# Kernel tuning notes

Measured on AMD Instinct MI355X. Metric: run time of the kernel, lower is better.

The kernel has to match this reference:

```python
import jax, jax.numpy as jnp
import numpy as np

N_NODES = 50000
N_EDGES = 800000
C = 128
NEG_SLOPE = 0.01  # nn.LeakyReLU default


def _init_linear(key, fan_in, fan_out):
    kw, kb = jax.random.split(key)
    lim = 1.0 / np.sqrt(fan_in)
    W = jax.random.uniform(kw, (fan_in, fan_out), jnp.float32, -lim, lim)
    b = jax.random.uniform(kb, (fan_out,), jnp.float32, -lim, lim)
    return W, b


def setup_inputs() -> dict:
    key = jax.random.key(0)
    ks = jax.random.split(key, 10)
    x = jax.random.normal(ks[0], (N_NODES, C), jnp.float32)
    pos = jax.random.normal(ks[1], (N_NODES, 3), jnp.float32)
    edge_index = jax.random.randint(ks[2], (2, N_EDGES), 0, N_NODES, jnp.int64)
    # mlp_h: Linear(C,C) -> LeakyReLU -> Linear(C,3) -> Tanh
    Wh1, bh1 = _init_linear(ks[3], C, C)
    Wh2, bh2 = _init_linear(ks[4], C, 3)
    # mlp_f: Linear(C+3, C) -> LeakyReLU
    Wf, bf = _init_linear(ks[5], C + 3, C)
    # mlp_g: Linear(C,C) -> LeakyReLU -> Linear(C,C)
    Wg1, bg1 = _init_linear(ks[6], C, C)
    Wg2, bg2 = _init_linear(ks[7], C, C)
    return {"x": x, "pos": pos, "edge_index": edge_index,
            "Wh1": Wh1, "bh1": bh1, "Wh2": Wh2, "bh2": bh2,
            "Wf": Wf, "bf": bf,
            "Wg1": Wg1, "bg1": bg1, "Wg2": Wg2, "bg2": bg2}


def reference(x, pos, edge_index, Wh1, bh1, Wh2, bh2, Wf, bf, Wg1, bg1, Wg2, bg2):
    lrelu = lambda t: jax.nn.leaky_relu(t, NEG_SLOPE)
    # delta_i = tanh(mlp_h(x_i))  -> [N, 3]
    delta = jnp.tanh(lrelu(x @ Wh1 + bh1) @ Wh2 + bh2)
    src, dst = edge_index[0], edge_index[1]  # message j -> i (PyG convention)
    # per-edge relative position: pos_j - pos_i + delta_i  -> [E, 3]
    rel = pos[src] - pos[dst] + delta[dst]
    # per-edge message: mlp_f([rel, x_j])  -> [E, C]
    e = lrelu(jnp.concatenate([rel, x[src]], axis=-1) @ Wf + bf)
    # scatter-max aggregate over incoming edges per target node
    agg = jax.ops.segment_max(e, dst, num_segments=N_NODES)
    agg = jnp.where(jnp.isfinite(agg), agg, 0.0)  # empty segments -> 0
    # out_i = mlp_g(agg_i) + x_i
    out = lrelu(agg @ Wg1 + bg1) @ Wg2 + bg2 + x
    return out
```

## Files before the change

### kernel.cpp

```cpp
#include <hip/hip_runtime.h>
#include <cfloat>
#include <cmath>

#define NEG_SLOPE 0.01f

typedef __attribute__((ext_vector_type(8))) short short8;
typedef __attribute__((ext_vector_type(4))) float f32x4;

__device__ __forceinline__ float lrelu(float v) { return v >= 0.0f ? v : NEG_SLOPE * v; }

__device__ __forceinline__ ushort f2b(float f) {
    unsigned u = __float_as_uint(f);
    u += 0x7fffu + ((u >> 16) & 1u);
    return (ushort)(u >> 16);
}
__device__ __forceinline__ float b2f(ushort s) { return __uint_as_float(((unsigned)s) << 16); }

__device__ __forceinline__ void split8(const float* v, short8& hi, short8& lo) {
#pragma unroll
    for (int j = 0; j < 8; ++j) {
        ushort h = f2b(v[j]);
        hi[j] = (short)h;
        lo[j] = (short)f2b(v[j] - b2f(h));
    }
}

__global__ __launch_bounds__(256) void count_wprep_kernel(
    const int* __restrict__ ei, int* __restrict__ G, int E,
    const float* __restrict__ Wh1, const float* __restrict__ Wf,
    const float* __restrict__ Wg1, const float* __restrict__ Wg2,
    ushort* __restrict__ WT)
{
    __shared__ int cnt[256];
    const int t = threadIdx.x;
    const int b = blockIdx.x;

    {
        int tt = b * 256 + t;
        int mat = tt >> 14;
        int idx = tt & 16383;
        int n = idx >> 7, k = idx & 127;
        float v;
        if (mat == 0)      v = Wh1[k * 128 + n];
        else if (mat == 1) v = Wf[(k + 3) * 128 + n];
        else if (mat == 2) v = Wg1[k * 128 + n];
        else               v = Wg2[k * 128 + n];
        WT[(tt - idx) + n * 128 + k] = f2b(v);
    }

    cnt[t] = 0;
    __syncthreads();
    for (int e = b * 256 + t; e < E; e += 65536)
        atomicAdd(&cnt[ei[E + e] >> 8], 1);
    __syncthreads();
    G[b * 256 + t] = cnt[t];
}


#define GEMM_CORE_REG(ACC, AH, AL)                                              \
    {                                                                           \
        _Pragma("unroll")                                                       \
        for (int ks = 0; ks < 4; ++ks) {                                        \
            _Pragma("unroll")                                                   \
            for (int nt = 0; nt < 8; ++nt) {                                    \
                short8 bfr = *(const short8*)&Bs[(nt * 16 + ln) * 136 + ks * 32 + qd * 8]; \
                ACC[nt] = __builtin_amdgcn_mfma_f32_16x16x32_bf16(AL[ks], bfr, ACC[nt], 0, 0, 0); \
                ACC[nt] = __builtin_amdgcn_mfma_f32_16x16x32_bf16(AH[ks], bfr, ACC[nt], 0, 0, 0); \
            }                                                                   \
        }                                                                       \
    }

#define STAGE_B(WTP)                                                            \
    {                                                                           \
        _Pragma("unroll")                                                       \
        for (int i = 0; i < 8; ++i) {                                           \
            int c = tid + 256 * i;                                              \
            int r = c >> 4, col8 = (c & 15) * 8;                                \
            *(uint4*)&Bs[r * 136 + col8] = *(const uint4*)((WTP) + r * 128 + col8); \
        }                                                                       \
    }

__global__ __launch_bounds__(256, 4) void hy_scanpart_kernel(
    const int* __restrict__ ei, const int* __restrict__ G,
    int* __restrict__ bbase, uint* __restrict__ bpairs, int E, int GB,
    const float* __restrict__ x, const ushort* __restrict__ WT,
    const float* __restrict__ bh1, const float* __restrict__ Wh2,
    const float* __restrict__ bh2, const float* __restrict__ Wf,
    const float* __restrict__ pos, float* __restrict__ q,
    ushort* __restrict__ yb, int M)
{
    __shared__ ushort Bs[128 * 136];
    __shared__ int sp[512];
    const int tid = threadIdx.x;

    if (blockIdx.x >= GB) {
        int* s   = sp;
        int* cur = sp + 256;
        const int b = blockIdx.x - GB;
        const int t = tid;

        int cs = 0, pp = 0;
        for (int bb = 0; bb < 256; ++bb) {
            int v = G[bb * 256 + t];
            if (bb < b) pp += v;
            cs += v;
        }
        s[t] = cs;
        __syncthreads();
        for (int d = 1; d < 256; d <<= 1) {
            int a = (t >= d) ? s[t - d] : 0;
            __syncthreads();
            s[t] += a;
            __syncthreads();
        }
        int colbase = s[t] - cs;
        cur[t] = colbase + pp;
        if (b == 0) {
            bbase[t] = colbase;
            if (t == 255) bbase[256] = colbase + cs;
        }
        __syncthreads();

        for (int e = b * 256 + t; e < E; e += 65536) {
            int src = ei[e];
            int dst = ei[E + e];
            int p = atomicAdd(&cur[dst >> 8], 1);
            bpairs[p] = (uint)src | ((uint)(dst & 255) << 24);
        }
        return;
    }

    const int w = tid >> 6, L = tid & 63, qd = L >> 4, ln = L & 15;
    const int row0 = blockIdx.x * 64;
    const int arow = row0 + w * 16 + ln;

    short8 ah[4], al[4];
    {
        const float* base = x + (size_t)((arow < M) ? arow : 0) * 128 + qd * 8;
        float vb[8];
#pragma unroll
        for (int ks = 0; ks < 4; ++ks) {
            float4 v0 = make_float4(0.f, 0.f, 0.f, 0.f), v1 = v0;
            if (arow < M) {
                v0 = *(const float4*)(base + ks * 32);
                v1 = *(const float4*)(base + ks * 32 + 4);
            }
            vb[0] = v0.x; vb[1] = v0.y; vb[2] = v0.z; vb[3] = v0.w;
            vb[4] = v1.x; vb[5] = v1.y; vb[6] = v1.z; vb[7] = v1.w;
            split8(vb, ah[ks], al[ks]);
        }
    }

    STAGE_B(WT);
    __syncthreads();
    f32x4 acc1[8];
#pragma unroll
    for (int nt = 0; nt < 8; ++nt) acc1[nt] = (f32x4){0.f, 0.f, 0.f, 0.f};
    GEMM_CORE_REG(acc1, ah, al);
    __syncthreads();

    STAGE_B(WT + 16384);
    __syncthreads();
    f32x4 acc2[8];
#pragma unroll
    for (int nt = 0; nt < 8; ++nt) acc2[nt] = (f32x4){0.f, 0.f, 0.f, 0.f};
    GEMM_CORE_REG(acc2, ah, al);

    float qa0[4], qa1[4], qa2[4];
#pragma unroll
    for (int r = 0; r < 4; ++r) { qa0[r] = 0.f; qa1[r] = 0.f; qa2[r] = 0.f; }
#pragma unroll
    for (int nt = 0; nt < 8; ++nt) {
        int nn = nt * 16 + ln;
        float bias = bh1[nn];
        float w0 = Wh2[nn * 3], w1 = Wh2[nn * 3 + 1], w2 = Wh2[nn * 3 + 2];
#pragma unroll
        for (int r = 0; r < 4; ++r) {
            float h = lrelu(acc1[nt][r] + bias);
            qa0[r] += h * w0; qa1[r] += h * w1; qa2[r] += h * w2;
        }
    }

    __syncthreads();

    ushort* ysS = (ushort*)Bs;
#pragma unroll
    for (int r = 0; r < 4; ++r) {
        int m = w * 16 + qd * 4 + r;
        int gm = row0 + m;
        float p0 = 0.f, p1 = 0.f, p2 = 0.f;
        if (gm < M) { p0 = pos[gm * 3]; p1 = pos[gm * 3 + 1]; p2 = pos[gm * 3 + 2]; }
#pragma unroll
        for (int nt = 0; nt < 8; ++nt) {
            int n = nt * 16 + ln;
            ysS[m * 128 + n] = f2b(acc2[nt][r] + p0 * Wf[n] + p1 * Wf[128 + n] + p2 * Wf[256 + n]);
        }
    }
    __syncthreads();

#pragma unroll
    for (int i = 0; i < 4; ++i) {
        int c = tid + 256 * i;
        int r = c >> 4, col8 = (c & 15) * 8;
        if (row0 + r < M)
            *(uint4*)(yb + (size_t)(row0 + r) * 128 + col8) = *(const uint4*)&ysS[r * 128 + col8];
    }

#pragma unroll
    for (int r = 0; r < 4; ++r) {
#pragma unroll
        for (int d = 1; d < 16; d <<= 1) {
            qa0[r] += __shfl_xor(qa0[r], d);
            qa1[r] += __shfl_xor(qa1[r], d);
            qa2[r] += __shfl_xor(qa2[r], d);
        }
    }
#pragma unroll
    for (int r = 0; r < 4; ++r) {
        int gm = row0 + w * 16 + qd * 4 + r;
        if (ln < 3 && gm < M) {
            float sv = (ln == 0) ? qa0[r] : (ln == 1) ? qa1[r] : qa2[r];
            q[gm * 3 + ln] = tanhf(sv + bh2[ln]) - pos[gm * 3 + ln];
        }
    }
}

__global__ __launch_bounds__(256) void bucket_csr_kernel(
    const uint* __restrict__ bpairs, const int* __restrict__ bbase,
    int* __restrict__ offs, int* __restrict__ srcs, int E, int M, int NBK)
{
    __shared__ int deg[256], scn[256], cur[256];
    const int b = blockIdx.x;
    const int t = threadIdx.x;
    const int base = bbase[b];
    const int end  = bbase[b + 1];
    deg[t] = 0;
    __syncthreads();
    for (int p = base + t; p < end; p += 256)
        atomicAdd(&deg[bpairs[p] >> 24], 1);
    __syncthreads();
    scn[t] = deg[t];
    __syncthreads();
    for (int d = 1; d < 256; d <<= 1) {
        int a = (t >= d) ? scn[t - d] : 0;
        __syncthreads();
        scn[t] += a;
        __syncthreads();
    }
    int excl = scn[t] - deg[t];
    cur[t] = excl;
    int node = b * 256 + t;
    if (node < M) offs[node] = base + excl;
    if (node == M - 1 || (b == NBK - 1 && t == 255)) offs[M] = E;
    __syncthreads();
    for (int p = base + t; p < end; p += 256) {
        uint pk = bpairs[p];
        int qpos = atomicAdd(&cur[pk >> 24], 1);
        srcs[base + qpos] = (int)(pk & 0xFFFFFFu);
    }
}

__global__ __launch_bounds__(256) void agg_kernel(
    const int* __restrict__ offs, const int* __restrict__ srcs,
    const ushort* __restrict__ yb, ushort* __restrict__ aggb, int M)
{
    int wave = threadIdx.x >> 6;
    int lane = threadIdx.x & 63;
    int node = blockIdx.x * 4 + wave;
    if (node >= M) return;
    int o0 = offs[node], o1 = offs[node + 1];
    float a0 = -INFINITY, a1 = -INFINITY;
    const uint* yp = (const uint*)yb;
    int j = o0;
    for (; j + 7 < o1; j += 8) {
        uint u[8];
#pragma unroll
        for (int t = 0; t < 8; ++t)
            u[t] = yp[(size_t)srcs[j + t] * 64 + lane];
#pragma unroll
        for (int t = 0; t < 8; ++t) {
            a0 = fmaxf(a0, __uint_as_float(u[t] << 16));
            a1 = fmaxf(a1, __uint_as_float(u[t] & 0xFFFF0000u));
        }
    }
    for (; j + 3 < o1; j += 4) {
        uint u[4];
#pragma unroll
        for (int t = 0; t < 4; ++t)
            u[t] = yp[(size_t)srcs[j + t] * 64 + lane];
#pragma unroll
        for (int t = 0; t < 4; ++t) {
            a0 = fmaxf(a0, __uint_as_float(u[t] << 16));
            a1 = fmaxf(a1, __uint_as_float(u[t] & 0xFFFF0000u));
        }
    }
    for (; j < o1; ++j) {
        uint u = yp[(size_t)srcs[j] * 64 + lane];
        a0 = fmaxf(a0, __uint_as_float(u << 16));
        a1 = fmaxf(a1, __uint_as_float(u & 0xFFFF0000u));
    }
    uint pk = (__float_as_uint(a0) >> 16) | (__float_as_uint(a1) & 0xFFFF0000u);
    ((uint*)aggb)[(size_t)node * 64 + lane] = pk;
}

__global__ __launch_bounds__(256) void midout_kernel(
    const ushort* __restrict__ aggb, const float* __restrict__ qv,
    const float* __restrict__ Wf, const float* __restrict__ bfv,
    const ushort* __restrict__ Wg1T, const float* __restrict__ bg1,
    const ushort* __restrict__ Wg2T, const float* __restrict__ bg2,
    const float* __restrict__ x, float* __restrict__ out, int M)
{
    __shared__ ushort Bs[128 * 136];
    __shared__ ushort Ms[64 * 136];
    const int tid = threadIdx.x;
    const int w = tid >> 6, L = tid & 63, qd = L >> 4, ln = L & 15;
    const int row0 = blockIdx.x * 64;
    const int arow = row0 + w * 16 + ln;

    short8 ah[4], al[4];
    {
        bool ok = arow < M;
        const ushort* base = aggb + (size_t)(ok ? arow : 0) * 128 + qd * 8;
        float q0 = 0.f, q1 = 0.f, q2 = 0.f;
        if (ok) { q0 = qv[arow * 3]; q1 = qv[arow * 3 + 1]; q2 = qv[arow * 3 + 2]; }
        float vb[8];
#pragma unroll
        for (int ks = 0; ks < 4; ++ks) {
            union { uint4 u; ushort s[8]; } a;
            a.u = ok ? *(const uint4*)(base + ks * 32) : make_uint4(0xFF80FF80u, 0xFF80FF80u, 0xFF80FF80u, 0xFF80FF80u);
#pragma unroll
            for (int j = 0; j < 8; ++j) {
                int k = ks * 32 + qd * 8 + j;
                float dec = 0.f;
                if (a.s[j] != 0xFF80u)
                    dec = lrelu(b2f(a.s[j]) + q0 * Wf[k] + q1 * Wf[128 + k] + q2 * Wf[256 + k] + bfv[k]);
                vb[j] = dec;
            }
            split8(vb, ah[ks], al[ks]);
        }
    }

    STAGE_B(Wg1T);
    __syncthreads();
    f32x4 macc[8];
#pragma unroll
    for (int nt = 0; nt < 8; ++nt) macc[nt] = (f32x4){0.f, 0.f, 0.f, 0.f};
    GEMM_CORE_REG(macc, ah, al);
    __syncthreads();

#pragma unroll
    for (int nt = 0; nt < 8; ++nt) {
        int n = nt * 16 + ln;
        float bias = bg1[n];
#pragma unroll
        for (int r = 0; r < 4; ++r)
            Ms[(w * 16 + qd * 4 + r) * 136 + n] = f2b(lrelu(macc[nt][r] + bias));
    }
    STAGE_B(Wg2T);
    __syncthreads();

    short8 a2[4];
#pragma unroll
    for (int ks = 0; ks < 4; ++ks)
        a2[ks] = *(const short8*)&Ms[(w * 16 + ln) * 136 + ks * 32 + qd * 8];

    f32x4 acc2[8];
#pragma unroll
    for (int nt = 0; nt < 8; ++nt) acc2[nt] = (f32x4){0.f, 0.f, 0.f, 0.f};
#pragma unroll
    for (int ks = 0; ks < 4; ++ks) {
#pragma unroll
        for (int nt = 0; nt < 8; ++nt) {
            short8 bfr = *(const short8*)&Bs[(nt * 16 + ln) * 136 + ks * 32 + qd * 8];
            acc2[nt] = __builtin_amdgcn_mfma_f32_16x16x32_bf16(a2[ks], bfr, acc2[nt], 0, 0, 0);
        }
    }
    __syncthreads();

    float* outS = (float*)Bs;
#pragma unroll
    for (int r = 0; r < 4; ++r) {
        int m = w * 16 + qd * 4 + r;
#pragma unroll
        for (int nt = 0; nt < 8; ++nt)
            outS[m * 132 + nt * 16 + ln] = acc2[nt][r];
    }
    __syncthreads();
#pragma unroll
    for (int i = 0; i < 8; ++i) {
        int c = tid + 256 * i;
        int r = c >> 5, col4 = (c & 31) * 4;
        int gr = row0 + r;
        if (gr < M) {
            float4 o = *(const float4*)&outS[r * 132 + col4];
            float4 bv = *(const float4*)(bg2 + col4);
            float4 xv = *(const float4*)(x + (size_t)gr * 128 + col4);
            o.x += bv.x + xv.x; o.y += bv.y + xv.y;
            o.z += bv.z + xv.z; o.w += bv.w + xv.w;
            *(float4*)(out + (size_t)gr * 128 + col4) = o;
        }
    }
}

extern "C" void kernel_launch(void* const* d_in, const int* in_sizes, int n_in,
                              void* d_out, int out_size, void* d_ws, size_t ws_size,
                              hipStream_t stream)
{
    const float* x   = (const float*)d_in[0];
    const float* pos = (const float*)d_in[1];
    const int*   ei  = (const int*)d_in[2];
    const float* Wh1 = (const float*)d_in[3];
    const float* bh1 = (const float*)d_in[4];
    const float* Wh2 = (const float*)d_in[5];
    const float* bh2 = (const float*)d_in[6];
    const float* Wf  = (const float*)d_in[7];
    const float* bf  = (const float*)d_in[8];
    const float* Wg1 = (const float*)d_in[9];
    const float* bg1 = (const float*)d_in[10];
    const float* Wg2 = (const float*)d_in[11];
    const float* bg2 = (const float*)d_in[12];
    float* out = (float*)d_out;

    const int M = in_sizes[0] / 128;
    const int E = in_sizes[2] / 2;
    const int NBK = (M + 255) >> 8;

    char* ws = (char*)d_ws;
    size_t off = 0;
    auto alloc = [&](size_t bytes) { void* p = ws + off; off += (bytes + 255) & ~255ull; return p; };
    ushort* yb     = (ushort*)alloc((size_t)M * 128 * sizeof(ushort));
    ushort* aggb   = (ushort*)alloc((size_t)M * 128 * sizeof(ushort));
    ushort* WT     = (ushort*)alloc(4 * 16384 * sizeof(ushort));
    float*  q      = (float*)alloc((size_t)M * 3 * sizeof(float));
    int*    offs   = (int*)alloc((size_t)(M + 1) * sizeof(int));
    int*    G      = (int*)alloc(256 * 256 * sizeof(int));
    int*    bbase  = (int*)alloc(257 * sizeof(int));
    uint*   bpairs = (uint*)alloc((size_t)E * sizeof(uint));
    int*    srcs   = (int*)alloc((size_t)E * sizeof(int));

    const int gb = (M + 63) / 64;

    count_wprep_kernel<<<256, 256, 0, stream>>>(ei, G, E, Wh1, Wf, Wg1, Wg2, WT);
    hy_scanpart_kernel<<<gb + 256, 256, 0, stream>>>(
        ei, G, bbase, bpairs, E, gb,
        x, WT, bh1, Wh2, bh2, Wf, pos, q, yb, M);
    bucket_csr_kernel<<<NBK, 256, 0, stream>>>(bpairs, bbase, offs, srcs, E, M, NBK);
    agg_kernel<<<(M + 3) / 4, 256, 0, stream>>>(offs, srcs, yb, aggb, M);
    midout_kernel<<<gb, 256, 0, stream>>>(aggb, q, Wf, bf,
                                          WT + 2 * 16384, bg1,
                                          WT + 3 * 16384, bg2, x, out, M);
}
```

Measured before the change: 208.2 us.

## Split scan-partition out of fused hy kernel and enlarge hy blocks

The scan/partition work moves out of the combined hy_scanpart kernel into its own scan_partition_kernel, launched after hy_kernel. Its column-sum loop is now split into prefix and suffix sums, unrolled by eight. hy_kernel becomes a 512-thread block covering 128 rows, with a matching weight-staging macro, intended to cut the number of weight loads and remove branch divergence between roles. In exchange, the scan work no longer overlaps the GEMM blocks. The tight launch bounds may also force register pressure or spills in the GEMM path.

```diff
diff --git a/kernel.cpp b/kernel.cpp
--- a/kernel.cpp
+++ b/kernel.cpp
@@ -56,6 +56,59 @@
     G[b * 256 + t] = cnt[t];
 }
 
+__global__ __launch_bounds__(256) void scan_partition_kernel(
+    const int* __restrict__ ei, const int* __restrict__ G,
+    int* __restrict__ bbase, uint* __restrict__ bpairs, int E)
+{
+    __shared__ int s[256];
+    __shared__ int cur[256];
+    const int b = blockIdx.x;
+    const int t = threadIdx.x;
+
+    int pp = 0, cs = 0;
+    int bb = 0;
+    for (; bb + 8 <= b; bb += 8) {
+        int v0 = G[(bb + 0) * 256 + t], v1 = G[(bb + 1) * 256 + t];
+        int v2 = G[(bb + 2) * 256 + t], v3 = G[(bb + 3) * 256 + t];
+        int v4 = G[(bb + 4) * 256 + t], v5 = G[(bb + 5) * 256 + t];
+        int v6 = G[(bb + 6) * 256 + t], v7 = G[(bb + 7) * 256 + t];
+        pp += ((v0 + v1) + (v2 + v3)) + ((v4 + v5) + (v6 + v7));
+    }
+    for (; bb < b; ++bb) pp += G[bb * 256 + t];
+    cs = pp;
+    for (; bb + 8 <= 256; bb += 8) {
+        int v0 = G[(bb + 0) * 256 + t], v1 = G[(bb + 1) * 256 + t];
+        int v2 = G[(bb + 2) * 256 + t], v3 = G[(bb + 3) * 256 + t];
+        int v4 = G[(bb + 4) * 256 + t], v5 = G[(bb + 5) * 256 + t];
+        int v6 = G[(bb + 6) * 256 + t], v7 = G[(bb + 7) * 256 + t];
+        cs += ((v0 + v1) + (v2 + v3)) + ((v4 + v5) + (v6 + v7));
+    }
+    for (; bb < 256; ++bb) cs += G[bb * 256 + t];
+
+    s[t] = cs;
+    __syncthreads();
+    for (int d = 1; d < 256; d <<= 1) {
+        int a = (t >= d) ? s[t - d] : 0;
+        __syncthreads();
+        s[t] += a;
+        __syncthreads();
+    }
+    int colbase = s[t] - cs;
+    cur[t] = colbase + pp;
+    if (b == 0) {
+        bbase[t] = colbase;
+        if (t == 255) bbase[256] = colbase + cs;
+    }
+    __syncthreads();
+
+    for (int e = b * 256 + t; e < E; e += 65536) {
+        int src = ei[e];
+        int dst = ei[E + e];
+        int p = atomicAdd(&cur[dst >> 8], 1);
+        bpairs[p] = (uint)src | ((uint)(dst & 255) << 24);
+    }
+}
+
 
 #define GEMM_CORE_REG(ACC, AH, AL)                                              \
     {                                                                           \
@@ -70,7 +123,7 @@
         }                                                                       \
     }
 
-#define STAGE_B(WTP)                                                            \
+#define STAGE_B256(WTP)                                                         \
     {                                                                           \
         _Pragma("unroll")                                                       \
         for (int i = 0; i < 8; ++i) {                                           \
@@ -79,10 +132,17 @@
             *(uint4*)&Bs[r * 136 + col8] = *(const uint4*)((WTP) + r * 128 + col8); \
         }                                                                       \
     }
-
-__global__ __launch_bounds__(256, 4) void hy_scanpart_kernel(
-    const int* __restrict__ ei, const int* __restrict__ G,
-    int* __restrict__ bbase, uint* __restrict__ bpairs, int E, int GB,
+#define STAGE_B512(WTP)                                                         \
+    {                                                                           \
+        _Pragma("unroll")                                                       \
+        for (int i = 0; i < 4; ++i) {                                           \
+            int c = tid + 512 * i;                                              \
+            int r = c >> 4, col8 = (c & 15) * 8;                                \
+            *(uint4*)&Bs[r * 136 + col8] = *(const uint4*)((WTP) + r * 128 + col8); \
+        }                                                                       \
+    }
+
+__global__ __launch_bounds__(512, 8) void hy_kernel(
     const float* __restrict__ x, const ushort* __restrict__ WT,
     const float* __restrict__ bh1, const float* __restrict__ Wh2,
     const float* __restrict__ bh2, const float* __restrict__ Wf,
@@ -90,48 +150,9 @@
     ushort* __restrict__ yb, int M)
 {
     __shared__ ushort Bs[128 * 136];
-    __shared__ int sp[512];
     const int tid = threadIdx.x;
-
-    if (blockIdx.x >= GB) {
-        int* s   = sp;
-        int* cur = sp + 256;
-        const int b = blockIdx.x - GB;
-        const int t = tid;
-
-        int cs = 0, pp = 0;
-        for (int bb = 0; bb < 256; ++bb) {
-            int v = G[bb * 256 + t];
-            if (bb < b) pp += v;
-            cs += v;
-        }
-        s[t] = cs;
-        __syncthreads();
-        for (int d = 1; d < 256; d <<= 1) {
-            int a = (t >= d) ? s[t - d] : 0;
-            __syncthreads();
-            s[t] += a;
-            __syncthreads();
-        }
-        int colbase = s[t] - cs;
-        cur[t] = colbase + pp;
-        if (b == 0) {
-            bbase[t] = colbase;
-            if (t == 255) bbase[256] = colbase + cs;
-        }
-        __syncthreads();
-
-        for (int e = b * 256 + t; e < E; e += 65536) {
-            int src = ei[e];
-            int dst = ei[E + e];
-            int p = atomicAdd(&cur[dst >> 8], 1);
-            bpairs[p] = (uint)src | ((uint)(dst & 255) << 24);
-        }
-        return;
-    }
-
     const int w = tid >> 6, L = tid & 63, qd = L >> 4, ln = L & 15;
-    const int row0 = blockIdx.x * 64;
+    const int row0 = blockIdx.x * 128;
     const int arow = row0 + w * 16 + ln;
 
     short8 ah[4], al[4];
@@ -151,7 +172,7 @@
         }
     }
 
-    STAGE_B(WT);
+    STAGE_B512(WT);
     __syncthreads();
     f32x4 acc1[8];
 #pragma unroll
@@ -159,7 +180,7 @@
     GEMM_CORE_REG(acc1, ah, al);
     __syncthreads();
 
-    STAGE_B(WT + 16384);
+    STAGE_B512(WT + 16384);
     __syncthreads();
     f32x4 acc2[8];
 #pragma unroll
@@ -200,7 +221,7 @@
 
 #pragma unroll
     for (int i = 0; i < 4; ++i) {
-        int c = tid + 256 * i;
+        int c = tid + 512 * i;
         int r = c >> 4, col8 = (c & 15) * 8;
         if (row0 + r < M)
             *(uint4*)(yb + (size_t)(row0 + r) * 128 + col8) = *(const uint4*)&ysS[r * 128 + col8];
@@ -340,7 +361,7 @@
         }
     }
 
-    STAGE_B(Wg1T);
+    STAGE_B256(Wg1T);
     __syncthreads();
     f32x4 macc[8];
 #pragma unroll
@@ -356,7 +377,7 @@
         for (int r = 0; r < 4; ++r)
             Ms[(w * 16 + qd * 4 + r) * 136 + n] = f2b(lrelu(macc[nt][r] + bias));
     }
-    STAGE_B(Wg2T);
+    STAGE_B256(Wg2T);
     __syncthreads();
 
     short8 a2[4];
@@ -438,15 +459,15 @@
     uint*   bpairs = (uint*)alloc((size_t)E * sizeof(uint));
     int*    srcs   = (int*)alloc((size_t)E * sizeof(int));
 
-    const int gb = (M + 63) / 64;
+    const int gbh = (M + 127) / 128;
+    const int gbm = (M + 63) / 64;
 
     count_wprep_kernel<<<256, 256, 0, stream>>>(ei, G, E, Wh1, Wf, Wg1, Wg2, WT);
-    hy_scanpart_kernel<<<gb + 256, 256, 0, stream>>>(
-        ei, G, bbase, bpairs, E, gb,
-        x, WT, bh1, Wh2, bh2, Wf, pos, q, yb, M);
+    hy_kernel<<<gbh, 512, 0, stream>>>(x, WT, bh1, Wh2, bh2, Wf, pos, q, yb, M);
+    scan_partition_kernel<<<256, 256, 0, stream>>>(ei, G, bbase, bpairs, E);
     bucket_csr_kernel<<<NBK, 256, 0, stream>>>(bpairs, bbase, offs, srcs, E, M, NBK);
     agg_kernel<<<(M + 3) / 4, 256, 0, stream>>>(offs, srcs, yb, aggb, M);
-    midout_kernel<<<gb, 256, 0, stream>>>(aggb, q, Wf, bf,
-                                          WT + 2 * 16384, bg1,
-                                          WT + 3 * 16384, bg2, x, out, M);
-}
+    midout_kernel<<<gbm, 256, 0, stream>>>(aggb, q, Wf, bf,
+                                           WT + 2 * 16384, bg1,
+                                           WT + 3 * 16384, bg2, x, out, M);
+}
```

After: 236.0 us. 1.13x slower.
